# Kernel tuning notes

Measured on AMD Instinct MI355X. Metric: run time of the kernel, lower is better.

## Reference

```python
import jax, jax.numpy as jnp
import numpy as np

N, E, T, F, HID, NCLS = 50000, 800000, 6, 64, 48, 2
LN_EPS = 1e-5


def setup_inputs() -> dict:
    key = jax.random.key(0)
    ks = jax.random.split(key, 24)
    p = lambda k, shape, s=0.1: jax.random.normal(k, shape, dtype=jnp.float32) * s
    inp = {
        "x_seq": jax.random.normal(ks[0], (T, N, F), dtype=jnp.float32),
        "edge_index": jax.random.randint(ks[1], (2, E), 0, N, dtype=jnp.int64),
        "edge_weight": jax.random.uniform(ks[2], (E,), dtype=jnp.float32),
        # GCN layer 0
        "W0": p(ks[3], (F, HID)), "b0": jnp.zeros((HID,), jnp.float32),
        "g0": jnp.ones((HID,), jnp.float32), "be0": jnp.zeros((HID,), jnp.float32),
        # GCN layer 1
        "W1": p(ks[4], (HID, HID)), "b1": jnp.zeros((HID,), jnp.float32),
        "g1": jnp.ones((HID,), jnp.float32), "be1": jnp.zeros((HID,), jnp.float32),
        # GRU (torch gate order: r, z, n)
        "W_ih": p(ks[5], (3 * HID, HID)), "W_hh": p(ks[6], (3 * HID, HID)),
        "b_ih": jnp.zeros((3 * HID,), jnp.float32), "b_hh": jnp.zeros((3 * HID,), jnp.float32),
        # classifier MLP
        "Wc1": p(ks[7], (HID, HID // 2)), "bc1": jnp.zeros((HID // 2,), jnp.float32),
        "Wc2": p(ks[8], (HID // 2, NCLS)), "bc2": jnp.zeros((NCLS,), jnp.float32),
    }
    return inp


def _layer_norm(x, g, b):
    mu = x.mean(-1, keepdims=True)
    var = ((x - mu) ** 2).mean(-1, keepdims=True)
    return (x - mu) * jax.lax.rsqrt(var + LN_EPS) * g + b


def reference(x_seq, edge_index, edge_weight, W0, b0, g0, be0, W1, b1, g1, be1,
              W_ih, W_hh, b_ih, b_hh, Wc1, bc1, Wc2, bc2):
    n = x_seq.shape[1]
    hid = W0.shape[1]
    row, col = edge_index[0], edge_index[1]
    # PyG GCNConv default: add self-loops (weight 1), symmetric normalization
    loop = jnp.arange(n)
    row_f = jnp.concatenate([row, loop])
    col_f = jnp.concatenate([col, loop])
    w_f = jnp.concatenate([edge_weight, jnp.ones((n,), edge_weight.dtype)])
    deg = jax.ops.segment_sum(w_f, col_f, num_segments=n)
    dis = jnp.where(deg > 0, jax.lax.rsqrt(jnp.maximum(deg, 1e-12)), 0.0)
    norm = dis[row_f] * w_f * dis[col_f]  # [E+N]

    def gcn(x, W, b):
        h = x @ W                              # [N, hid]
        msg = h[row_f] * norm[:, None]         # [E+N, hid]
        return jax.ops.segment_sum(msg, col_f, num_segments=n) + b

    def spatial(x_t):
        # layer 0: no residual (in_dim != hid)
        h1 = jax.nn.relu(_layer_norm(gcn(x_t, W0, b0), g0, be0))
        # layer 1: residual (dropout is eval-mode no-op)
        h2 = jax.nn.relu(_layer_norm(gcn(h1, W1, b1), g1, be1)) + h1
        return h2

    # sequential map over T keeps per-step [E,hid] message buffers small
    H = jax.lax.map(spatial, x_seq)            # [T, N, hid]

    def gru_step(h, x_t):
        gi = x_t @ W_ih.T + b_ih               # [N, 3*hid]
        gh = h @ W_hh.T + b_hh
        i_r, i_z, i_n = jnp.split(gi, 3, axis=-1)
        h_r, h_z, h_n = jnp.split(gh, 3, axis=-1)
        r = jax.nn.sigmoid(i_r + h_r)
        z = jax.nn.sigmoid(i_z + h_z)
        nv = jnp.tanh(i_n + r * h_n)
        h_new = (1.0 - z) * nv + z * h
        return h_new, None

    h0 = jnp.zeros((n, hid), x_seq.dtype)
    z_last, _ = jax.lax.scan(gru_step, h0, H)  # last hidden state [N, hid]

    logits = jax.nn.relu(z_last @ Wc1 + bc1) @ Wc2 + bc2  # [N, 2]
    return logits
```

## Files before the change

### kernel.cpp

```cpp
#include <hip/hip_runtime.h>
#include <hip/hip_fp16.h>
#include <math.h>

#define NN 50000
#define NE 800000
#define TT 6
#define HID 48
#define NB 196

__device__ __forceinline__ float sigmoidf_(float x){ return 1.0f/(1.0f+__expf(-x)); }
__device__ __forceinline__ float tanhf_(float x){
  float xc = fminf(fmaxf(x,-15.f),15.f);
  float t = __expf(2.f*xc);
  return (t-1.f)/(t+1.f);
}
__device__ __forceinline__ unsigned f2bf(float x){
  unsigned u = __float_as_uint(x);
  return (u + 0x7fffu + ((u>>16)&1u)) >> 16;
}
__device__ __forceinline__ unsigned pack2(float a, float b){
  return f2bf(a) | (f2bf(b)<<16);
}
__device__ __forceinline__ float bflo(unsigned u){ return __uint_as_float(u<<16); }
__device__ __forceinline__ float bfhi(unsigned u){ return __uint_as_float(u & 0xffff0000u); }
__device__ __forceinline__ unsigned f2h(float x){
  return (unsigned)__half_as_ushort(__float2half(x));
}
__device__ __forceinline__ float h2f(unsigned u){
  return __half2float(__ushort_as_half((unsigned short)(u & 0xffffu)));
}
__device__ __forceinline__ unsigned pack2h(float a, float b){
  return f2h(a) | (f2h(b)<<16);
}

typedef __fp16 h2t __attribute__((ext_vector_type(2)));

__device__ __forceinline__ unsigned pkrtz(float a, float b){
#if __has_builtin(__builtin_amdgcn_cvt_pkrtz)
  auto r = __builtin_amdgcn_cvt_pkrtz(a, b);
  return __builtin_bit_cast(unsigned, r);
#else
  return pack2h(a, b);
#endif
}
__device__ __forceinline__ float dot2f(unsigned a, unsigned b, float c){
#if __has_builtin(__builtin_amdgcn_fdot2)
  return __builtin_amdgcn_fdot2(__builtin_bit_cast(h2t, a), __builtin_bit_cast(h2t, b), c, false);
#else
  h2t av = __builtin_bit_cast(h2t, a), bv = __builtin_bit_cast(h2t, b);
  return c + (float)av[0]*(float)bv[0] + (float)av[1]*(float)bv[1];
#endif
}

struct U3 { unsigned x,y,z; };

__device__ __forceinline__ int block_scan_incl(int x, int* wsum){
  int lane = threadIdx.x & 63, w = threadIdx.x >> 6;
  int v = x;
#pragma unroll
  for(int d=1; d<64; d<<=1){
    int u = __shfl_up(v, d, 64);
    if(lane >= d) v += u;
  }
  if(lane==63) wsum[w] = v;
  __syncthreads();
  int add = 0;
#pragma unroll
  for(int k=0;k<3;k++) if(w>k) add += wsum[k];
  return v + add;
}

__global__ __launch_bounds__(256) void k_setup(int* cnt,
                                               const float* __restrict__ Wih, const float* __restrict__ Whh,
                                               unsigned* Wall){
  int i = blockIdx.x*256+threadIdx.x;
  if(i<NN) cnt[i]=0;
  if(i < 6*24*48){
    int wv = i/1152, r = i%1152;
    int k2 = r/48, c = r%48;
    int cc = (c<24)? c : (c-24);
    int row = (cc<8) ? (wv*8 + cc) : (cc<16) ? (48 + wv*8 + cc-8) : (96 + wv*8 + cc-16);
    const float* Wsrc = (c<24)? Whh : Wih;
    Wall[i] = pack2h(Wsrc[row*48 + 2*k2], Wsrc[row*48 + 2*k2 + 1]);
  }
}

__global__ __launch_bounds__(256) void k_cnt(const int* __restrict__ ei, int* cnt, int* pos){
  int e = blockIdx.x*256+threadIdx.x;
  if(e<NE){
    int c = ei[NE+e];
    pos[e] = atomicAdd(&cnt[c], 1);
  }
}

__global__ __launch_bounds__(256) void k_partA(const int* __restrict__ cnt, int* bsum){
  __shared__ int wsum[4];
  int i = blockIdx.x*256+threadIdx.x;
  int x = (i<NN)? cnt[i] : 0;
  int lane = threadIdx.x & 63, w = threadIdx.x >> 6;
  int v = x;
#pragma unroll
  for(int m=32;m>=1;m>>=1) v += __shfl_xor(v, m, 64);
  if(lane==0) wsum[w]=v;
  __syncthreads();
  if(threadIdx.x==0) bsum[blockIdx.x] = wsum[0]+wsum[1]+wsum[2]+wsum[3];
}

__global__ __launch_bounds__(256) void k_midB(const int* __restrict__ bsum, int* bpre, int* offs){
  __shared__ int wsum[4];
  int t = threadIdx.x;
  int x = (t<NB)? bsum[t] : 0;
  int incl = block_scan_incl(x, wsum);
  if(t<NB) bpre[t] = incl - x;
  if(t==255) offs[NN] = incl;
}

__global__ __launch_bounds__(256) void k_offsC(const int* __restrict__ cnt, const int* __restrict__ bpre,
                                               int* offs){
  __shared__ int wsum[4];
  int i = blockIdx.x*256+threadIdx.x;
  int x = (i<NN)? cnt[i] : 0;
  int incl = block_scan_incl(x, wsum);
  if(i<NN) offs[i] = bpre[blockIdx.x] + incl - x;
}

__global__ __launch_bounds__(256) void k_scatter(const int* __restrict__ ei, const float* __restrict__ ew,
                                                 const int* __restrict__ offs, const int* __restrict__ pos,
                                                 int2* __restrict__ csr){
  int e = blockIdx.x*256+threadIdx.x;
  if(e<NE){
    int c = ei[NE+e];
    int2 v; v.x = ei[e]; v.y = __float_as_int(ew[e]);
    csr[offs[c]+pos[e]] = v;
  }
}

__global__ __launch_bounds__(256) void k_deg(const int2* __restrict__ csr, const int* __restrict__ offs,
                                             float* dis){
  int i = blockIdx.x*256+threadIdx.x;
  if(i<NN){
    float s = 1.f;
    int e0=offs[i], e1=offs[i+1];
    for(int j=e0;j<e1;j++) s += __int_as_float(csr[j].y);
    dis[i] = rsqrtf(s);
  }
}

__global__ __launch_bounds__(256) void k_normE(int2* __restrict__ csr, const float* __restrict__ dis){
  int j = blockIdx.x*256+threadIdx.x;
  if(j<NE){
    int2 v = csr[j];
    v.y = __float_as_int(dis[v.x]*__int_as_float(v.y));
    csr[j] = v;
  }
}

__global__ __launch_bounds__(256) void k_mm0(const float* __restrict__ X, const float* __restrict__ W,
                                             unsigned* __restrict__ A){
  int s = __builtin_amdgcn_readfirstlane(threadIdx.x>>6);
  int n = blockIdx.x*64 + (threadIdx.x&63);
  if(n>=NN) return;
  const float* xb = X + (long long)n*64;
  const float* wb = W + 12*s;
  float acc[TT][12];
#pragma unroll
  for(int t=0;t<TT;t++)
#pragma unroll
    for(int j=0;j<12;j++) acc[t][j]=0.f;
#pragma unroll 2
  for(int k4=0;k4<16;k4++){
    float4 xv[TT];
#pragma unroll
    for(int t=0;t<TT;t++) xv[t] = *reinterpret_cast<const float4*>(xb + (long long)t*NN*64 + 4*k4);
#pragma unroll
    for(int q=0;q<4;q++){
      const float* wr = wb + (4*k4+q)*HID;
      float w[12];
#pragma unroll
      for(int j=0;j<12;j++) w[j]=wr[j];
#pragma unroll
      for(int t=0;t<TT;t++){
        float xs = (&xv[t].x)[q];
#pragma unroll
        for(int j=0;j<12;j++) acc[t][j] = fmaf(xs, w[j], acc[t][j]);
      }
    }
  }
  unsigned buf[36];
#pragma unroll
  for(int j=0;j<12;j++){
    buf[3*j  ]=pack2(acc[0][j],acc[1][j]);
    buf[3*j+1]=pack2(acc[2][j],acc[3][j]);
    buf[3*j+2]=pack2(acc[4][j],acc[5][j]);
  }
  uint4* o4 = reinterpret_cast<uint4*>(A + (long long)n*144 + 36*s);
#pragma unroll
  for(int q=0;q<9;q++) o4[q] = make_uint4(buf[4*q],buf[4*q+1],buf[4*q+2],buf[4*q+3]);
}

__global__ __launch_bounds__(256) void k_mm1(const float* __restrict__ X, const float* __restrict__ W,
                                             unsigned* __restrict__ A){
  int s = __builtin_amdgcn_readfirstlane(threadIdx.x>>6);
  int n = blockIdx.x*64 + (threadIdx.x&63);
  if(n>=NN) return;
  const float* xb = X + (long long)n*(TT*HID);
  const float* wb = W + 12*s;
  float acc[TT][12];
#pragma unroll
  for(int t=0;t<TT;t++)
#pragma unroll
    for(int j=0;j<12;j++) acc[t][j]=0.f;
#pragma unroll 2
  for(int k4=0;k4<12;k4++){
    float4 xv[TT];
#pragma unroll
    for(int t=0;t<TT;t++) xv[t] = *reinterpret_cast<const float4*>(xb + t*HID + 4*k4);
#pragma unroll
    for(int q=0;q<4;q++){
      const float* wr = wb + (4*k4+q)*HID;
      float w[12];
#pragma unroll
      for(int j=0;j<12;j++) w[j]=wr[j];
#pragma unroll
      for(int t=0;t<TT;t++){
        float xs = (&xv[t].x)[q];
#pragma unroll
        for(int j=0;j<12;j++) acc[t][j] = fmaf(xs, w[j], acc[t][j]);
      }
    }
  }
  unsigned buf[36];
#pragma unroll
  for(int j=0;j<12;j++){
    buf[3*j  ]=pack2(acc[0][j],acc[1][j]);
    buf[3*j+1]=pack2(acc[2][j],acc[3][j]);
    buf[3*j+2]=pack2(acc[4][j],acc[5][j]);
  }
  uint4* o4 = reinterpret_cast<uint4*>(A + (long long)n*144 + 36*s);
#pragma unroll
  for(int q=0;q<9;q++) o4[q] = make_uint4(buf[4*q],buf[4*q+1],buf[4*q+2],buf[4*q+3]);
}

__global__ __launch_bounds__(256) void k_agg(const unsigned* __restrict__ A, const float* __restrict__ bias,
                                             const float* __restrict__ gain, const float* __restrict__ beta,
                                             const float* __restrict__ resid, float* __restrict__ out,
                                             const int* __restrict__ offs, const int2* __restrict__ csr,
                                             const float* __restrict__ dis){
  int wid = (blockIdx.x*256+threadIdx.x)>>6;
  int lane = threadIdx.x & 63;
  if(wid>=NN) return;
  const bool act = lane<HID;
  const int f = act? lane : (HID-1);
  float dn = dis[wid];
  float acc[TT];
  {
    U3 v = *reinterpret_cast<const U3*>(A + (long long)wid*144 + 3*f);
    acc[0]=dn*bflo(v.x); acc[1]=dn*bfhi(v.x);
    acc[2]=dn*bflo(v.y); acc[3]=dn*bfhi(v.y);
    acc[4]=dn*bflo(v.z); acc[5]=dn*bfhi(v.z);
  }
  int e0=offs[wid], e1=offs[wid+1];
  int e=e0;
  for(; e+3<e1; e+=4){
    int2 i0=csr[e], i1=csr[e+1], i2=csr[e+2], i3=csr[e+3];
    U3 d0 = *reinterpret_cast<const U3*>(A + (long long)i0.x*144 + 3*f);
    U3 d1 = *reinterpret_cast<const U3*>(A + (long long)i1.x*144 + 3*f);
    U3 d2 = *reinterpret_cast<const U3*>(A + (long long)i2.x*144 + 3*f);
    U3 d3 = *reinterpret_cast<const U3*>(A + (long long)i3.x*144 + 3*f);
    float n0=__int_as_float(i0.y), n1=__int_as_float(i1.y);
    float n2=__int_as_float(i2.y), n3=__int_as_float(i3.y);
    acc[0]=fmaf(n0,bflo(d0.x),acc[0]); acc[1]=fmaf(n0,bfhi(d0.x),acc[1]);
    acc[2]=fmaf(n0,bflo(d0.y),acc[2]); acc[3]=fmaf(n0,bfhi(d0.y),acc[3]);
    acc[4]=fmaf(n0,bflo(d0.z),acc[4]); acc[5]=fmaf(n0,bfhi(d0.z),acc[5]);
    acc[0]=fmaf(n1,bflo(d1.x),acc[0]); acc[1]=fmaf(n1,bfhi(d1.x),acc[1]);
    acc[2]=fmaf(n1,bflo(d1.y),acc[2]); acc[3]=fmaf(n1,bfhi(d1.y),acc[3]);
    acc[4]=fmaf(n1,bflo(d1.z),acc[4]); acc[5]=fmaf(n1,bfhi(d1.z),acc[5]);
    acc[0]=fmaf(n2,bflo(d2.x),acc[0]); acc[1]=fmaf(n2,bfhi(d2.x),acc[1]);
    acc[2]=fmaf(n2,bflo(d2.y),acc[2]); acc[3]=fmaf(n2,bfhi(d2.y),acc[3]);
    acc[4]=fmaf(n2,bflo(d2.z),acc[4]); acc[5]=fmaf(n2,bfhi(d2.z),acc[5]);
    acc[0]=fmaf(n3,bflo(d3.x),acc[0]); acc[1]=fmaf(n3,bfhi(d3.x),acc[1]);
    acc[2]=fmaf(n3,bflo(d3.y),acc[2]); acc[3]=fmaf(n3,bfhi(d3.y),acc[3]);
    acc[4]=fmaf(n3,bflo(d3.z),acc[4]); acc[5]=fmaf(n3,bfhi(d3.z),acc[5]);
  }
  for(; e<e1; ++e){
    int2 i0=csr[e];
    U3 d0 = *reinterpret_cast<const U3*>(A + (long long)i0.x*144 + 3*f);
    float n0=__int_as_float(i0.y);
    acc[0]=fmaf(n0,bflo(d0.x),acc[0]); acc[1]=fmaf(n0,bfhi(d0.x),acc[1]);
    acc[2]=fmaf(n0,bflo(d0.y),acc[2]); acc[3]=fmaf(n0,bfhi(d0.y),acc[3]);
    acc[4]=fmaf(n0,bflo(d0.z),acc[4]); acc[5]=fmaf(n0,bfhi(d0.z),acc[5]);
  }
  float bb = bias[f], gg = gain[f], be = beta[f];
  const float rn = 1.0f/HID;
#pragma unroll
  for(int t=0;t<TT;t++){
    float val = fmaf(acc[t], dn, bb);
    float v = act? val : 0.f;
    float s = v, s2 = v*v;
#pragma unroll
    for(int m=32;m>=1;m>>=1){
      s  += __shfl_xor(s,  m, 64);
      s2 += __shfl_xor(s2, m, 64);
    }
    float mu  = s*rn;
    float var = fmaxf(s2*rn - mu*mu, 0.f);
    float y = (val-mu)*rsqrtf(var+1e-5f)*gg + be;
    y = fmaxf(y, 0.f);
    long long oidx = (long long)wid*(TT*HID) + t*HID + f;
    if(resid) y += resid[oidx];
    if(act) out[oidx] = y;
  }
}

__global__ __launch_bounds__(384) void k_gruF2(const float* __restrict__ X,
                                               const unsigned* __restrict__ Wall,
                                               const float* __restrict__ bih, const float* __restrict__ bhh,
                                               const float* __restrict__ Wc1, const float* __restrict__ bc1,
                                               const float* __restrict__ Wc2, const float* __restrict__ bc2,
                                               float* __restrict__ out){
  __shared__ unsigned xall[TT*24*64];
  __shared__ unsigned hb[2][24*64];
  int tid = threadIdx.x;
  int wv = __builtin_amdgcn_readfirstlane(tid>>6);
  int lane = tid & 63;
  int f0 = wv*8;
  long long n = (long long)blockIdx.x*64 + lane;
  long long gn = (n<NN)? n : (NN-1);

  {
    const float* xb = X + gn*(TT*HID) + wv*HID;
#pragma unroll
    for(int q=0;q<12;q++){
      float4 v = *reinterpret_cast<const float4*>(xb + 4*q);
      xall[(wv*24 + 2*q  )*64 + lane] = pkrtz(v.x, v.y);
      xall[(wv*24 + 2*q+1)*64 + lane] = pkrtz(v.z, v.w);
    }
  }
  for(int i=tid;i<24*64;i+=384) hb[0][i]=0u;

  float rb[8], zb[8], nbi[8], nbh[8], hprev[8];
#pragma unroll
  for(int j=0;j<8;j++){
    rb[j] = bih[f0+j]    + bhh[f0+j];
    zb[j] = bih[48+f0+j] + bhh[48+f0+j];
    nbi[j]= bih[96+f0+j];
    nbh[j]= bhh[96+f0+j];
    hprev[j]=0.f;
  }
  __syncthreads();

  int cur=0;
  for(int t=0;t<TT;t++){
    float acc[24], accn[8];
#pragma unroll
    for(int j=0;j<8;j++){ acc[j]=rb[j]; acc[8+j]=zb[j]; acc[16+j]=nbh[j]; accn[j]=nbi[j]; }
    const unsigned* hbc = &hb[cur][0];
    const unsigned* xtc = &xall[t*24*64];
#pragma unroll 2
    for(int k2=0;k2<24;k2++){
      const unsigned* wp = Wall + (wv*24+k2)*48;
      unsigned ws[48];
#pragma unroll
      for(int q=0;q<48;q++) ws[q]=wp[q];
      unsigned h2k = hbc[k2*64+lane];
      unsigned xk  = xtc[k2*64+lane];
#pragma unroll
      for(int c=0;c<24;c++) acc[c]  = dot2f(h2k, ws[c],    acc[c]);
#pragma unroll
      for(int c=0;c<16;c++) acc[c]  = dot2f(xk,  ws[24+c], acc[c]);
#pragma unroll
      for(int c=0;c<8;c++)  accn[c] = dot2f(xk,  ws[40+c], accn[c]);
    }
    unsigned* hw = &hb[cur^1][0];
    float hn[8];
#pragma unroll
    for(int j=0;j<8;j++){
      float r  = sigmoidf_(acc[j]);
      float zg = sigmoidf_(acc[8+j]);
      float ng = tanhf_(accn[j] + r*acc[16+j]);
      float hv = (1.f-zg)*ng + zg*hprev[j];
      hprev[j]=hv; hn[j]=hv;
    }
#pragma unroll
    for(int m=0;m<4;m++) hw[(wv*4+m)*64+lane] = pack2h(hn[2*m], hn[2*m+1]);
    __syncthreads();
    cur^=1;
  }

  if(wv==0 && n<NN){
    const unsigned* hbc=&hb[cur][0];
    float hv[24];
#pragma unroll
    for(int j=0;j<24;j++) hv[j]=bc1[j];
#pragma unroll 2
    for(int k2=0;k2<24;k2++){
      unsigned u = hbc[k2*64+lane];
      float hk0 = h2f(u), hk1 = h2f(u>>16);
      const float* w0 = Wc1 + (2*k2)*24;
      const float* w1 = Wc1 + (2*k2+1)*24;
#pragma unroll
      for(int j=0;j<24;j++) hv[j] = fmaf(hk0, w0[j], hv[j]);
#pragma unroll
      for(int j=0;j<24;j++) hv[j] = fmaf(hk1, w1[j], hv[j]);
    }
    float l0=bc2[0], l1=bc2[1];
#pragma unroll
    for(int j=0;j<24;j++){
      float a = fmaxf(hv[j],0.f);
      l0 = fmaf(a, Wc2[2*j],   l0);
      l1 = fmaf(a, Wc2[2*j+1], l1);
    }
    reinterpret_cast<float2*>(out)[n] = make_float2(l0,l1);
  }
}

static inline size_t al256(size_t x){ return (x+255)&~(size_t)255; }

extern "C" void kernel_launch(void* const* d_in, const int* in_sizes, int n_in,
                              void* d_out, int out_size, void* d_ws, size_t ws_size,
                              hipStream_t stream){
  const float* x_seq=(const float*)d_in[0];
  const int*   ei   =(const int*)d_in[1];
  const float* ew   =(const float*)d_in[2];
  const float* W0=(const float*)d_in[3];  const float* b0=(const float*)d_in[4];
  const float* g0=(const float*)d_in[5];  const float* be0=(const float*)d_in[6];
  const float* W1=(const float*)d_in[7];  const float* b1=(const float*)d_in[8];
  const float* g1=(const float*)d_in[9];  const float* be1=(const float*)d_in[10];
  const float* Wih=(const float*)d_in[11];const float* Whh=(const float*)d_in[12];
  const float* bih=(const float*)d_in[13];const float* bhh=(const float*)d_in[14];
  const float* Wc1=(const float*)d_in[15];const float* bc1=(const float*)d_in[16];
  const float* Wc2=(const float*)d_in[17];const float* bc2=(const float*)d_in[18];
  float* outp=(float*)d_out;

  char* p=(char*)d_ws; size_t off=0;
  auto alloc=[&](size_t bytes)->void*{ void* r=p+off; off=al256(off+bytes); return r; };
  float* dis    =(float*)alloc((size_t)NN*4);
  int*   cnt    =(int*)  alloc((size_t)NN*4);
  int*   offs   =(int*)  alloc((size_t)(NN+1)*4);
  int*   bsum   =(int*)  alloc((size_t)NB*4);
  int*   bpre   =(int*)  alloc((size_t)NB*4);
  int*   pos    =(int*)  alloc((size_t)NE*4);
  int2*  csr    =(int2*) alloc((size_t)NE*8);
  unsigned* Wall=(unsigned*)alloc((size_t)6*24*48*4);
  unsigned* A   =(unsigned*)alloc((size_t)NN*576 + 1024);
  float* h1     =(float*)alloc((size_t)NN*TT*HID*4);
  float* h2     =(float*)alloc((size_t)NN*TT*HID*4);

  const int GN=(NN+255)/256, GE=(NE+255)/256;
  const int GMM=(NN+63)/64;
  const int GAGG=(NN*64+255)/256;
  const int GGRU=(NN+63)/64;

  k_setup  <<<GN,256,0,stream>>>(cnt,Wih,Whh,Wall);
  k_cnt    <<<GE,256,0,stream>>>(ei,cnt,pos);
  k_partA  <<<NB,256,0,stream>>>(cnt,bsum);
  k_midB   <<<1,256,0,stream>>>(bsum,bpre,offs);
  k_offsC  <<<NB,256,0,stream>>>(cnt,bpre,offs);
  k_scatter<<<GE,256,0,stream>>>(ei,ew,offs,pos,csr);
  k_deg    <<<GN,256,0,stream>>>(csr,offs,dis);
  k_normE  <<<GE,256,0,stream>>>(csr,dis);

  k_mm0<<<GMM,256,0,stream>>>(x_seq, W0, A);
  k_agg<<<GAGG,256,0,stream>>>(A,b0,g0,be0,nullptr,h1,offs,csr,dis);
  k_mm1<<<GMM,256,0,stream>>>(h1, W1, A);
  k_agg<<<GAGG,256,0,stream>>>(A,b1,g1,be1,h1,h2,offs,csr,dis);
  k_gruF2<<<GGRU,384,0,stream>>>(h2, Wall, bih,bhh, Wc1,bc1,Wc2,bc2, outp);
}
```

Before: 694.5 us.

## Stage GRU weights in LDS and double-buffer per-timestep input loads

The GRU kernel now copies the packed recurrent and input weights into shared memory once per block and reads them as 128-bit LDS loads, replacing per-iteration global/scalar loads. Input activations are no longer loaded for all timesteps up front. Each step prefetches the next timestep's inputs into registers with coalesced float4 loads and writes them into a padded double buffer before the barrier, overlapping global latency with the matvec. The trade-off is a larger shared-memory footprint (about 27KB of weights), which can reduce occupancy, plus extra LDS traffic for the broadcast weight reads.

```diff
diff --git a/kernel.cpp b/kernel.cpp
--- a/kernel.cpp
+++ b/kernel.cpp
@@ -312,31 +312,42 @@
   }
 }
 
-__global__ __launch_bounds__(384) void k_gruF2(const float* __restrict__ X,
+__global__ __launch_bounds__(384) void k_gruF3(const float* __restrict__ X,
                                                const unsigned* __restrict__ Wall,
                                                const float* __restrict__ bih, const float* __restrict__ bhh,
                                                const float* __restrict__ Wc1, const float* __restrict__ bc1,
                                                const float* __restrict__ Wc2, const float* __restrict__ bc2,
                                                float* __restrict__ out){
-  __shared__ unsigned xall[TT*24*64];
+  __shared__ __align__(16) unsigned Wl[6*24*48];
+  __shared__ unsigned xb[2][24*66];
   __shared__ unsigned hb[2][24*64];
   int tid = threadIdx.x;
   int wv = __builtin_amdgcn_readfirstlane(tid>>6);
   int lane = tid & 63;
   int f0 = wv*8;
   long long n = (long long)blockIdx.x*64 + lane;
-  long long gn = (n<NN)? n : (NN-1);
 
   {
-    const float* xb = X + gn*(TT*HID) + wv*HID;
-#pragma unroll
-    for(int q=0;q<12;q++){
-      float4 v = *reinterpret_cast<const float4*>(xb + 4*q);
-      xall[(wv*24 + 2*q  )*64 + lane] = pkrtz(v.x, v.y);
-      xall[(wv*24 + 2*q+1)*64 + lane] = pkrtz(v.z, v.w);
-    }
+    const uint4* wsrc = reinterpret_cast<const uint4*>(Wall);
+    uint4* wdst = reinterpret_cast<uint4*>(Wl);
+    for(int i=tid;i<1728;i+=384) wdst[i]=wsrc[i];
   }
   for(int i=tid;i<24*64;i+=384) hb[0][i]=0u;
+
+  int c0 = tid, c1 = tid+384;
+  int nd0 = c0/12, q0 = c0-12*nd0;
+  int nd1 = c1/12, q1 = c1-12*nd1;
+  long long g0 = (long long)blockIdx.x*64+nd0; if(g0>NN-1) g0=NN-1;
+  long long g1 = (long long)blockIdx.x*64+nd1; if(g1>NN-1) g1=NN-1;
+  const float* xs0 = X + g0*(TT*HID);
+  const float* xs1 = X + g1*(TT*HID);
+  {
+    float4 v0 = *reinterpret_cast<const float4*>(xs0 + 4*q0);
+    float4 v1 = *reinterpret_cast<const float4*>(xs1 + 4*q1);
+    int b0 = (2*q0)*66+nd0, b1 = (2*q1)*66+nd1;
+    xb[0][b0]=pkrtz(v0.x,v0.y); xb[0][b0+66]=pkrtz(v0.z,v0.w);
+    xb[0][b1]=pkrtz(v1.x,v1.y); xb[0][b1+66]=pkrtz(v1.z,v1.w);
+  }
 
   float rb[8], zb[8], nbi[8], nbh[8], hprev[8];
 #pragma unroll
@@ -351,19 +362,27 @@
 
   int cur=0;
   for(int t=0;t<TT;t++){
+    float4 xv0, xv1;
+    if(t<TT-1){
+      xv0 = *reinterpret_cast<const float4*>(xs0 + (t+1)*HID + 4*q0);
+      xv1 = *reinterpret_cast<const float4*>(xs1 + (t+1)*HID + 4*q1);
+    }
     float acc[24], accn[8];
 #pragma unroll
     for(int j=0;j<8;j++){ acc[j]=rb[j]; acc[8+j]=zb[j]; acc[16+j]=nbh[j]; accn[j]=nbi[j]; }
     const unsigned* hbc = &hb[cur][0];
-    const unsigned* xtc = &xall[t*24*64];
+    const unsigned* xtc = &xb[t&1][0];
 #pragma unroll 2
     for(int k2=0;k2<24;k2++){
-      const unsigned* wp = Wall + (wv*24+k2)*48;
+      const uint4* wr4 = reinterpret_cast<const uint4*>(Wl + (wv*24+k2)*48);
       unsigned ws[48];
 #pragma unroll
-      for(int q=0;q<48;q++) ws[q]=wp[q];
+      for(int q=0;q<12;q++){
+        uint4 w = wr4[q];
+        ws[4*q]=w.x; ws[4*q+1]=w.y; ws[4*q+2]=w.z; ws[4*q+3]=w.w;
+      }
       unsigned h2k = hbc[k2*64+lane];
-      unsigned xk  = xtc[k2*64+lane];
+      unsigned xk  = xtc[k2*66+lane];
 #pragma unroll
       for(int c=0;c<24;c++) acc[c]  = dot2f(h2k, ws[c],    acc[c]);
 #pragma unroll
@@ -383,6 +402,12 @@
     }
 #pragma unroll
     for(int m=0;m<4;m++) hw[(wv*4+m)*64+lane] = pack2h(hn[2*m], hn[2*m+1]);
+    if(t<TT-1){
+      unsigned* xw = &xb[(t+1)&1][0];
+      int b0 = (2*q0)*66+nd0, b1 = (2*q1)*66+nd1;
+      xw[b0]=pkrtz(xv0.x,xv0.y); xw[b0+66]=pkrtz(xv0.z,xv0.w);
+      xw[b1]=pkrtz(xv1.x,xv1.y); xw[b1+66]=pkrtz(xv1.z,xv1.w);
+    }
     __syncthreads();
     cur^=1;
   }
@@ -464,5 +489,5 @@
   k_agg<<<GAGG,256,0,stream>>>(A,b0,g0,be0,nullptr,h1,offs,csr,dis);
   k_mm1<<<GMM,256,0,stream>>>(h1, W1, A);
   k_agg<<<GAGG,256,0,stream>>>(A,b1,g1,be1,h1,h2,offs,csr,dis);
-  k_gruF2<<<GGRU,384,0,stream>>>(h2, Wall, bih,bhh, Wc1,bc1,Wc2,bc2, outp);
-}
+  k_gruF3<<<GGRU,384,0,stream>>>(h2, Wall, bih,bhh, Wc1,bc1,Wc2,bc2, outp);
+}
```

After: 726.2 us. 1.05x slower.

## Compute degrees with atomics during counting and fold edge norm into scatter

Applied to the files above, without the earlier changes.

Degree sums are now accumulated with float atomicAdd in the counting kernel, and the rsqrt is folded into the partial-sum kernel. The source-side normalisation is applied while scattering into CSR, which removes the separate k_deg and k_normE passes and their extra reads and writes of the CSR array. The aggregation loop also gains an 8-wide unrolled gather stage to keep more loads in flight. Float atomics make the degree sums order-nondeterministic and add atomic traffic, and the wider unroll raises register pressure.

```diff
diff --git a/kernel.cpp b/kernel.cpp
--- a/kernel.cpp
+++ b/kernel.cpp
@@ -70,11 +70,11 @@
   return v + add;
 }
 
-__global__ __launch_bounds__(256) void k_setup(int* cnt,
+__global__ __launch_bounds__(256) void k_setup(int* cnt, float* degf,
                                                const float* __restrict__ Wih, const float* __restrict__ Whh,
                                                unsigned* Wall){
   int i = blockIdx.x*256+threadIdx.x;
-  if(i<NN) cnt[i]=0;
+  if(i<NN){ cnt[i]=0; degf[i]=0.f; }
   if(i < 6*24*48){
     int wv = i/1152, r = i%1152;
     int k2 = r/48, c = r%48;
@@ -85,18 +85,21 @@
   }
 }
 
-__global__ __launch_bounds__(256) void k_cnt(const int* __restrict__ ei, int* cnt, int* pos){
+__global__ __launch_bounds__(256) void k_cnt(const int* __restrict__ ei, const float* __restrict__ ew,
+                                             int* cnt, float* degf, int* pos){
   int e = blockIdx.x*256+threadIdx.x;
   if(e<NE){
     int c = ei[NE+e];
     pos[e] = atomicAdd(&cnt[c], 1);
-  }
-}
-
-__global__ __launch_bounds__(256) void k_partA(const int* __restrict__ cnt, int* bsum){
+    atomicAdd(&degf[c], ew[e]);
+  }
+}
+
+__global__ __launch_bounds__(256) void k_partA(const int* __restrict__ cnt, int* bsum, float* dis){
   __shared__ int wsum[4];
   int i = blockIdx.x*256+threadIdx.x;
   int x = (i<NN)? cnt[i] : 0;
+  if(i<NN) dis[i] = rsqrtf(1.f + dis[i]);
   int lane = threadIdx.x & 63, w = threadIdx.x >> 6;
   int v = x;
 #pragma unroll
@@ -126,32 +129,13 @@
 
 __global__ __launch_bounds__(256) void k_scatter(const int* __restrict__ ei, const float* __restrict__ ew,
                                                  const int* __restrict__ offs, const int* __restrict__ pos,
-                                                 int2* __restrict__ csr){
+                                                 const float* __restrict__ dis, int2* __restrict__ csr){
   int e = blockIdx.x*256+threadIdx.x;
   if(e<NE){
     int c = ei[NE+e];
-    int2 v; v.x = ei[e]; v.y = __float_as_int(ew[e]);
+    int r = ei[e];
+    int2 v; v.x = r; v.y = __float_as_int(dis[r]*ew[e]);
     csr[offs[c]+pos[e]] = v;
-  }
-}
-
-__global__ __launch_bounds__(256) void k_deg(const int2* __restrict__ csr, const int* __restrict__ offs,
-                                             float* dis){
-  int i = blockIdx.x*256+threadIdx.x;
-  if(i<NN){
-    float s = 1.f;
-    int e0=offs[i], e1=offs[i+1];
-    for(int j=e0;j<e1;j++) s += __int_as_float(csr[j].y);
-    dis[i] = rsqrtf(s);
-  }
-}
-
-__global__ __launch_bounds__(256) void k_normE(int2* __restrict__ csr, const float* __restrict__ dis){
-  int j = blockIdx.x*256+threadIdx.x;
-  if(j<NE){
-    int2 v = csr[j];
-    v.y = __float_as_int(dis[v.x]*__int_as_float(v.y));
-    csr[j] = v;
   }
 }
 
@@ -261,26 +245,35 @@
   }
   int e0=offs[wid], e1=offs[wid+1];
   int e=e0;
+  for(; e+7<e1; e+=8){
+    int2 ii[8];
+#pragma unroll
+    for(int u=0;u<8;u++) ii[u]=csr[e+u];
+    U3 dd[8];
+#pragma unroll
+    for(int u=0;u<8;u++) dd[u]=*reinterpret_cast<const U3*>(A + (long long)ii[u].x*144 + 3*f);
+#pragma unroll
+    for(int u=0;u<8;u++){
+      float nr=__int_as_float(ii[u].y);
+      acc[0]=fmaf(nr,bflo(dd[u].x),acc[0]); acc[1]=fmaf(nr,bfhi(dd[u].x),acc[1]);
+      acc[2]=fmaf(nr,bflo(dd[u].y),acc[2]); acc[3]=fmaf(nr,bfhi(dd[u].y),acc[3]);
+      acc[4]=fmaf(nr,bflo(dd[u].z),acc[4]); acc[5]=fmaf(nr,bfhi(dd[u].z),acc[5]);
+    }
+  }
   for(; e+3<e1; e+=4){
-    int2 i0=csr[e], i1=csr[e+1], i2=csr[e+2], i3=csr[e+3];
-    U3 d0 = *reinterpret_cast<const U3*>(A + (long long)i0.x*144 + 3*f);
-    U3 d1 = *reinterpret_cast<const U3*>(A + (long long)i1.x*144 + 3*f);
-    U3 d2 = *reinterpret_cast<const U3*>(A + (long long)i2.x*144 + 3*f);
-    U3 d3 = *reinterpret_cast<const U3*>(A + (long long)i3.x*144 + 3*f);
-    float n0=__int_as_float(i0.y), n1=__int_as_float(i1.y);
-    float n2=__int_as_float(i2.y), n3=__int_as_float(i3.y);
-    acc[0]=fmaf(n0,bflo(d0.x),acc[0]); acc[1]=fmaf(n0,bfhi(d0.x),acc[1]);
-    acc[2]=fmaf(n0,bflo(d0.y),acc[2]); acc[3]=fmaf(n0,bfhi(d0.y),acc[3]);
-    acc[4]=fmaf(n0,bflo(d0.z),acc[4]); acc[5]=fmaf(n0,bfhi(d0.z),acc[5]);
-    acc[0]=fmaf(n1,bflo(d1.x),acc[0]); acc[1]=fmaf(n1,bfhi(d1.x),acc[1]);
-    acc[2]=fmaf(n1,bflo(d1.y),acc[2]); acc[3]=fmaf(n1,bfhi(d1.y),acc[3]);
-    acc[4]=fmaf(n1,bflo(d1.z),acc[4]); acc[5]=fmaf(n1,bfhi(d1.z),acc[5]);
-    acc[0]=fmaf(n2,bflo(d2.x),acc[0]); acc[1]=fmaf(n2,bfhi(d2.x),acc[1]);
-    acc[2]=fmaf(n2,bflo(d2.y),acc[2]); acc[3]=fmaf(n2,bfhi(d2.y),acc[3]);
-    acc[4]=fmaf(n2,bflo(d2.z),acc[4]); acc[5]=fmaf(n2,bfhi(d2.z),acc[5]);
-    acc[0]=fmaf(n3,bflo(d3.x),acc[0]); acc[1]=fmaf(n3,bfhi(d3.x),acc[1]);
-    acc[2]=fmaf(n3,bflo(d3.y),acc[2]); acc[3]=fmaf(n3,bfhi(d3.y),acc[3]);
-    acc[4]=fmaf(n3,bflo(d3.z),acc[4]); acc[5]=fmaf(n3,bfhi(d3.z),acc[5]);
+    int2 ii[4];
+#pragma unroll
+    for(int u=0;u<4;u++) ii[u]=csr[e+u];
+    U3 dd[4];
+#pragma unroll
+    for(int u=0;u<4;u++) dd[u]=*reinterpret_cast<const U3*>(A + (long long)ii[u].x*144 + 3*f);
+#pragma unroll
+    for(int u=0;u<4;u++){
+      float nr=__int_as_float(ii[u].y);
+      acc[0]=fmaf(nr,bflo(dd[u].x),acc[0]); acc[1]=fmaf(nr,bfhi(dd[u].x),acc[1]);
+      acc[2]=fmaf(nr,bflo(dd[u].y),acc[2]); acc[3]=fmaf(nr,bfhi(dd[u].y),acc[3]);
+      acc[4]=fmaf(nr,bflo(dd[u].z),acc[4]); acc[5]=fmaf(nr,bfhi(dd[u].z),acc[5]);
+    }
   }
   for(; e<e1; ++e){
     int2 i0=csr[e];
@@ -451,14 +444,12 @@
   const int GAGG=(NN*64+255)/256;
   const int GGRU=(NN+63)/64;
 
-  k_setup  <<<GN,256,0,stream>>>(cnt,Wih,Whh,Wall);
-  k_cnt    <<<GE,256,0,stream>>>(ei,cnt,pos);
-  k_partA  <<<NB,256,0,stream>>>(cnt,bsum);
+  k_setup  <<<GN,256,0,stream>>>(cnt,dis,Wih,Whh,Wall);
+  k_cnt    <<<GE,256,0,stream>>>(ei,ew,cnt,dis,pos);
+  k_partA  <<<NB,256,0,stream>>>(cnt,bsum,dis);
   k_midB   <<<1,256,0,stream>>>(bsum,bpre,offs);
   k_offsC  <<<NB,256,0,stream>>>(cnt,bpre,offs);
-  k_scatter<<<GE,256,0,stream>>>(ei,ew,offs,pos,csr);
-  k_deg    <<<GN,256,0,stream>>>(csr,offs,dis);
-  k_normE  <<<GE,256,0,stream>>>(csr,dis);
+  k_scatter<<<GE,256,0,stream>>>(ei,ew,offs,pos,dis,csr);
 
   k_mm0<<<GMM,256,0,stream>>>(x_seq, W0, A);
   k_agg<<<GAGG,256,0,stream>>>(A,b0,g0,be0,nullptr,h1,offs,csr,dis);
```

New measurement: 727.1 us. 4.7% more time.
